# Performance work log

Measured on AMD Instinct MI355X. Metric: run time of the kernel, lower is better.

Reference implementation:

```python
import jax, jax.numpy as jnp
import numpy as np

B, T = 8, 1024
IN_FEAT = 1024
N_FEAT = 1024
N_HEAD = 16
D_K = N_FEAT // N_HEAD
KERNEL = 11
LEFT_PAD = (KERNEL - 1) // 2  # sanm_shift=0
RIGHT_PAD = KERNEL - 1 - LEFT_PAD


def setup_inputs() -> dict:
    key = jax.random.key(0)
    ks = jax.random.split(key, 7)
    hidden_states = jax.random.normal(ks[0], (B, T, IN_FEAT), dtype=jnp.float32)
    mask = jax.random.randint(ks[1], (B, 1, T), 0, 2, dtype=jnp.int32)
    s_qkv = 1.0 / np.sqrt(IN_FEAT)
    s_out = 1.0 / np.sqrt(N_FEAT)
    W_qkv = jax.random.normal(ks[2], (3 * N_FEAT, IN_FEAT), dtype=jnp.float32) * s_qkv
    b_qkv = jnp.zeros((3 * N_FEAT,), dtype=jnp.float32)
    W_out = jax.random.normal(ks[3], (N_FEAT, N_FEAT), dtype=jnp.float32) * s_out
    b_out = jnp.zeros((N_FEAT,), dtype=jnp.float32)
    fsmn_kernel = jax.random.normal(ks[4], (N_FEAT, 1, KERNEL), dtype=jnp.float32) * (1.0 / KERNEL)
    return {"hidden_states": hidden_states, "mask": mask, "W_qkv": W_qkv,
            "b_qkv": b_qkv, "W_out": W_out, "b_out": b_out, "fsmn_kernel": fsmn_kernel}


def _fsmn(v, maskf, fsmn_kernel):
    # v: [B,T,D], maskf: [B,T,1]
    vm = v * maskf
    x = jnp.transpose(vm, (0, 2, 1))  # [B,D,T]
    x = jnp.pad(x, ((0, 0), (0, 0), (LEFT_PAD, RIGHT_PAD)))
    # depthwise conv1d (cross-correlation, matching torch Conv1d)
    y = jax.lax.conv_general_dilated(
        x, fsmn_kernel, window_strides=(1,), padding='VALID',
        dimension_numbers=('NCH', 'OIH', 'NCH'), feature_group_count=N_FEAT)
    y = jnp.transpose(y, (0, 2, 1)) + vm  # [B,T,D]
    return y * maskf


def reference(hidden_states, mask, W_qkv, b_qkv, W_out, b_out, fsmn_kernel):
    b, t, _ = hidden_states.shape
    qkv = jnp.einsum('btf,of->bto', hidden_states, W_qkv) + b_qkv  # [B,T,3*N_FEAT]
    q, k, v = jnp.split(qkv, 3, axis=-1)
    def heads(x):
        return jnp.transpose(x.reshape(b, t, N_HEAD, D_K), (0, 2, 1, 3))  # [B,H,T,D_K]
    q_h, k_h, v_h = heads(q), heads(k), heads(v)

    maskf = mask.reshape(b, t, 1).astype(hidden_states.dtype)
    fsmn_memory = _fsmn(v, maskf, fsmn_kernel)

    scale = D_K ** -0.5
    scores = jnp.einsum('bhqd,bhkd->bhqk', q_h * scale, k_h)  # [B,H,T,T]
    mask_keys = (mask.reshape(b, 1, 1, t) == 0)  # True where padded
    scores = jnp.where(mask_keys, -jnp.inf, scores)
    attn = jax.nn.softmax(scores, axis=-1)
    attn = jnp.where(mask_keys, 0.0, attn)
    ctx = jnp.einsum('bhqk,bhkd->bhqd', attn, v_h)  # [B,H,T,D_K]
    ctx = jnp.transpose(ctx, (0, 2, 1, 3)).reshape(b, t, N_FEAT)
    att_outs = jnp.einsum('btf,of->bto', ctx, W_out) + b_out
    return att_outs + fsmn_memory
```

## Files before the change

kernel.cpp:

```cpp
#include <hip/hip_runtime.h>
#include <stdint.h>


typedef uint16_t u16;
typedef float f32x4 __attribute__((ext_vector_type(4)));
typedef __bf16 bf16x8 __attribute__((ext_vector_type(8)));
typedef __bf16 bf16x2 __attribute__((ext_vector_type(2)));
typedef u16 u16x8 __attribute__((ext_vector_type(8)));
typedef u16 u16x4 __attribute__((ext_vector_type(4)));
typedef short s16x4 __attribute__((ext_vector_type(4)));

__device__ __forceinline__ u16 f2bf(float f) {
    union { float f; uint32_t u; } c; c.f = f;
    uint32_t u = c.u;
    return (u16)((u + 0x7fffu + ((u >> 16) & 1u)) >> 16);
}
__device__ __forceinline__ float bf2f(u16 h) {
    union { uint32_t u; float f; } c; c.u = ((uint32_t)h) << 16;
    return c.f;
}
__device__ __forceinline__ uint32_t pack_bf16(float a, float b) {
    bf16x2 t; t[0] = (__bf16)a; t[1] = (__bf16)b;
    union { bf16x2 v; uint32_t u; } c; c.v = t; return c.u;
}

__global__ __launch_bounds__(256) void cvt_all(const float* __restrict__ hs,
                                               const float* __restrict__ wqkv,
                                               const float* __restrict__ wout,
                                               u16* __restrict__ hsb,
                                               u16* __restrict__ wqkvb,
                                               u16* __restrict__ woutb) {
    int bid = blockIdx.x;
    const float* src; u16* dst; int ib;
    if (bid < 8192)       { src = hs;   dst = hsb;   ib = bid; }
    else if (bid < 11264) { src = wqkv; dst = wqkvb; ib = bid - 8192; }
    else                  { src = wout; dst = woutb; ib = bid - 11264; }
    int i = (ib * 256 + threadIdx.x) * 4;
    float4 v = *reinterpret_cast<const float4*>(src + i);
    ushort4 o;
    o.x = f2bf(v.x); o.y = f2bf(v.y); o.z = f2bf(v.z); o.w = f2bf(v.w);
    *reinterpret_cast<ushort4*>(dst + i) = o;
}

__global__ void mask_and_kt(const int* __restrict__ mask, uint32_t* __restrict__ mb,
                            const float* __restrict__ fk, float* __restrict__ kt) {
    int bid = blockIdx.x;
    if (bid < 44) {
        int idx = bid * 256 + threadIdx.x;
        int j = idx >> 10, c = idx & 1023;
        kt[idx] = fk[c * 11 + j];
    } else {
        int i = threadIdx.x;
        int b = i >> 5, c = i & 31;
        uint32_t u = 0;
        for (int j = 0; j < 32; ++j)
            u |= (mask[(b << 10) + c * 32 + j] ? 1u : 0u) << j;
        mb[i] = u;
    }
}

__global__ __launch_bounds__(256) void transpose_v(const u16* __restrict__ vn,
                                                   u16* __restrict__ vt) {
    __shared__ u16 ts[64][68];
    const int tid = threadIdx.x;
    const int bh = blockIdx.x >> 4;
    const int kc = blockIdx.x & 15;
    const u16* src = vn + ((size_t)bh << 16) + (size_t)kc * 64 * 64;
#pragma unroll
    for (int it = 0; it < 2; ++it) {
        int ch = it * 256 + tid;
        int k = ch >> 3, g = ch & 7;
        *reinterpret_cast<u16x8*>(&ts[k][g * 8]) =
            *reinterpret_cast<const u16x8*>(src + k * 64 + g * 8);
    }
    __syncthreads();
    u16* dst = vt + ((size_t)bh << 16) + kc * 64;
#pragma unroll
    for (int it = 0; it < 2; ++it) {
        int ch = it * 256 + tid;
        int d = ch >> 3, gk = ch & 7;
        u16x8 v;
#pragma unroll
        for (int j = 0; j < 8; ++j) v[j] = ts[gk * 8 + j][d];
        *reinterpret_cast<u16x8*>(dst + (size_t)d * 1024 + gk * 8) = v;
    }
}

template<int MODE>
__global__ __launch_bounds__(512, 4) void gemm_bk32(
    const u16* __restrict__ A, const u16* __restrict__ Bw, int M, int N, int K,
    int ntiles_n, const float* __restrict__ bias,
    u16* __restrict__ qo, u16* __restrict__ ko, u16* __restrict__ vo,
    float* __restrict__ out)
{
    __shared__ u16 lds[36864];
    const int t = threadIdx.x;
    const int lane = t & 63;
    const int wave = t >> 6;
    const int wr = wave >> 2, wc = wave & 3;
    const int lr = lane & 15, lq = lane >> 4;
    const int r3 = lane >> 2, c4 = lane & 3;
    const int cpx = gridDim.x >> 3;
    const int bid = (blockIdx.x & 7) * cpx + (blockIdx.x >> 3);
    const int m0 = (bid / ntiles_n) * 128;
    const int n0 = (bid % ntiles_n) * 256;
    const int NT = K >> 5;

    const u16* AgW  = A  + (size_t)(m0 + wave * 16 + r3) * K + c4 * 8;
    const u16* BgW0 = Bw + (size_t)(n0 + wave * 16 + r3) * K + c4 * 8;
    const u16* BgW1 = BgW0 + (size_t)128 * K;

    auto stage = [&](int buf, int tile) {
        u16* dA  = lds + buf * 12288 + wave * 512;
        u16* dB0 = lds + buf * 12288 + 4096 + wave * 512;
        u16* dB1 = dB0 + 4096;
        __builtin_amdgcn_global_load_lds(
            (const __attribute__((address_space(1))) void*)(AgW + tile * 32),
            (__attribute__((address_space(3))) void*)dA, 16, 0, 0);
        __builtin_amdgcn_global_load_lds(
            (const __attribute__((address_space(1))) void*)(BgW0 + tile * 32),
            (__attribute__((address_space(3))) void*)dB0, 16, 0, 0);
        __builtin_amdgcn_global_load_lds(
            (const __attribute__((address_space(1))) void*)(BgW1 + tile * 32),
            (__attribute__((address_space(3))) void*)dB1, 16, 0, 0);
    };

    f32x4 acc[4][4];
#pragma unroll
    for (int i = 0; i < 4; ++i)
#pragma unroll
        for (int j = 0; j < 4; ++j) acc[i][j] = (f32x4){0.f, 0.f, 0.f, 0.f};

    stage(0, 0);
    stage(1, 1);
    asm volatile("s_waitcnt vmcnt(3)" ::: "memory");
    __builtin_amdgcn_s_barrier();

    for (int T = 0; T < NT; ++T) {
        const int bcur = T % 3;
        const u16* Ab = lds + bcur * 12288;
        const u16* Bb = Ab + 4096;
        bf16x8 a[4], bb[4];
#pragma unroll
        for (int mm = 0; mm < 4; ++mm)
            a[mm] = *reinterpret_cast<const bf16x8*>(Ab + (wr * 64 + mm * 16 + lr) * 32 + lq * 8);
#pragma unroll
        for (int nn = 0; nn < 4; ++nn)
            bb[nn] = *reinterpret_cast<const bf16x8*>(Bb + (wc * 64 + nn * 16 + lr) * 32 + lq * 8);
        if (T + 2 < NT) stage((T + 2) % 3, T + 2);
        __builtin_amdgcn_s_setprio(1);
#pragma unroll
        for (int mm = 0; mm < 4; ++mm)
#pragma unroll
            for (int nn = 0; nn < 4; ++nn)
                acc[mm][nn] = __builtin_amdgcn_mfma_f32_16x16x32_bf16(a[mm], bb[nn], acc[mm][nn], 0, 0, 0);
        __builtin_amdgcn_s_setprio(0);
        if (T + 2 < NT)      asm volatile("s_waitcnt vmcnt(3)" ::: "memory");
        else if (T + 1 < NT) asm volatile("s_waitcnt vmcnt(0)" ::: "memory");
        if (T + 1 < NT) __builtin_amdgcn_s_barrier();
    }

#pragma unroll
    for (int m = 0; m < 4; ++m) {
        int row = m0 + wr * 64 + m * 16 + lq * 4;
#pragma unroll
        for (int n = 0; n < 4; ++n) {
            int col = n0 + wc * 64 + n * 16 + lr;
            float bv = bias[col];
#pragma unroll
            for (int r = 0; r < 4; ++r) {
                float val = acc[m][n][r] + bv;
                int rr = row + r;
                if (MODE == 0) {
                    int part = col >> 10;
                    int cc = col & 1023;
                    int h = cc >> 6, d = cc & 63;
                    int b = rr >> 10, tt = rr & 1023;
                    size_t bh = (size_t)(b * 16 + h);
                    u16* dst = (part == 0) ? qo : (part == 1) ? ko : vo;
                    dst[((bh << 10) + tt) * 64 + d] = f2bf(part == 0 ? val * 0.18033688011f : val);
                } else {
                    size_t o = (size_t)rr * N + col;
                    out[o] += val;
                }
            }
        }
    }
}

__global__ __launch_bounds__(256) void fsmn_v3(const u16* __restrict__ vt,
                                               const int* __restrict__ mask,
                                               const float* __restrict__ kt,
                                               float* __restrict__ out)
{
    __shared__ float vs[64][147];
    __shared__ float ms[144];
    const int tid = threadIdx.x;
    const int tc = blockIdx.x & 7;
    const int bh = blockIdx.x >> 3;
    const int b = bh >> 4, h = bh & 15;
    const int t0 = tc * 128;
    const u16* vrow = vt + ((size_t)bh << 16);
    const int* mrow = mask + (b << 10);

    if (tid < 144) {
        int tt = t0 - 8 + tid;
        ms[tid] = (tt >= 0 && tt < 1024) ? (float)mrow[tt] : 0.f;
    }
    const int sd = tid >> 2;
    const int ci0 = tid & 3;
#pragma unroll
    for (int it = 0; it < 5; ++it) {
        int ci = ci0 + it * 4;
        if (ci < 18) {
            int tbase = t0 - 8 + ci * 8;
            if (tbase >= 0 && tbase < 1024) {
                u16x8 v8 = *reinterpret_cast<const u16x8*>(vrow + (size_t)sd * 1024 + tbase);
#pragma unroll
                for (int j = 0; j < 8; ++j)
                    vs[sd][ci * 8 + j] = bf2f((u16)v8[j]) * (float)mrow[tbase + j];
            } else {
#pragma unroll
                for (int j = 0; j < 8; ++j) vs[sd][ci * 8 + j] = 0.f;
            }
        }
    }
    __syncthreads();

    const int dd = tid & 63;
    const int tg = tid >> 6;
    const int c = h * 64 + dd;
    float kc[11];
#pragma unroll
    for (int j = 0; j < 11; ++j) kc[j] = kt[j * 1024 + c];

    const int tl0 = tg * 32;
    float w[11];
#pragma unroll
    for (int j = 0; j < 11; ++j) w[j] = vs[dd][3 + tl0 + j];
    float* orow = out + ((size_t)(b * 1024 + t0 + tl0)) * 1024 + c;
#pragma unroll 4
    for (int s = 0; s < 32; ++s) {
        float acc = 0.f;
#pragma unroll
        for (int j = 0; j < 11; ++j) acc += kc[j] * w[j];
        float mf = ms[8 + tl0 + s];
        orow[(size_t)s * 1024] = (acc + w[5]) * mf;
#pragma unroll
        for (int j = 0; j < 10; ++j) w[j] = w[j + 1];
        w[10] = vs[dd][3 + tl0 + s + 11];
    }
}

__global__ __launch_bounds__(512) void attn_v9(const u16* __restrict__ qg,
                                               const u16* __restrict__ kg,
                                               const u16* __restrict__ vtg,
                                               const uint32_t* __restrict__ mbits,
                                               u16* __restrict__ ctx)
{
    __shared__ u16 K_s[2][64 * 64];
    __shared__ u16 V_s[2][64 * 64];
    const int t = threadIdx.x;
    const int lane = t & 63;
    const int w = t >> 6;
    const int lr = lane & 15, lq = lane >> 4;
    const int bh = blockIdx.x & 127;
    const int qc = blockIdx.x >> 7;
    const int b = bh >> 4, h = bh & 15;
    const size_t base = (size_t)bh << 16;
    const u16* kb = kg + base;
    const u16* vb = vtg + base;
    const int q0 = qc * 256 + w * 32;

    bf16x8 qf[2][2];
#pragma unroll
    for (int qt = 0; qt < 2; ++qt)
#pragma unroll
        for (int kk = 0; kk < 2; ++kk)
            qf[qt][kk] = *reinterpret_cast<const bf16x8*>(
                qg + base + (size_t)(q0 + qt * 16 + lr) * 64 + kk * 32 + lq * 8);

    f32x4 oacc[2][4];
    f32x4 oacc_l[2];
#pragma unroll
    for (int qt = 0; qt < 2; ++qt) {
        oacc_l[qt] = (f32x4){0.f, 0.f, 0.f, 0.f};
#pragma unroll
        for (int dt = 0; dt < 4; ++dt) oacc[qt][dt] = (f32x4){0.f, 0.f, 0.f, 0.f};
    }

    s16x4 ones_f;
#pragma unroll
    for (int j = 0; j < 4; ++j) ones_f[j] = (short)0x3F80;

    const uint32_t* mrow = mbits + b * 32;

    auto stage = [&](int bufi, int tile) {
        const int k0s = tile * 64;
        int ch = w * 64 + lane;
        int row = ch >> 3, c7 = ch & 7;
        int sc = (c7 ^ (row & 7)) * 8;
        const u16* srcK = kb + (size_t)(k0s + row) * 64 + sc;
        const u16* srcV = vb + (size_t)row * 1024 + k0s + sc;
        u16* dK = &K_s[bufi][(size_t)(w * 64) * 8];
        u16* dV = &V_s[bufi][(size_t)(w * 64) * 8];
        __builtin_amdgcn_global_load_lds(
            (const __attribute__((address_space(1))) void*)srcK,
            (__attribute__((address_space(3))) void*)dK, 16, 0, 0);
        __builtin_amdgcn_global_load_lds(
            (const __attribute__((address_space(1))) void*)srcV,
            (__attribute__((address_space(3))) void*)dV, 16, 0, 0);
    };

    int cur = 0;
    stage(0, 0);
    asm volatile("s_waitcnt vmcnt(0)");
    __syncthreads();

    for (int it = 0; it < 16; ++it) {
        if (it < 15) stage(cur ^ 1, it + 1);

        const u16* Kb = K_s[cur];
        bf16x8 kf[4][2];
#pragma unroll
        for (int kt = 0; kt < 4; ++kt) {
            int row = kt * 16 + lr;
#pragma unroll
            for (int kk = 0; kk < 2; ++kk) {
                int g = (kk * 4 + lq) ^ (row & 7);
                kf[kt][kk] = *reinterpret_cast<const bf16x8*>(Kb + row * 64 + g * 8);
            }
        }

        const uint32_t mw0 = mrow[it * 2], mw1 = mrow[it * 2 + 1];
        uint32_t mb_[4];
        mb_[0] = mw0 >> (lq * 4);
        mb_[1] = mw0 >> (16 + lq * 4);
        mb_[2] = mw1 >> (lq * 4);
        mb_[3] = mw1 >> (16 + lq * 4);
        f32x4 ma[4];
#pragma unroll
        for (int kt = 0; kt < 4; ++kt)
#pragma unroll
            for (int r = 0; r < 4; ++r)
                ma[kt][r] = (mb_[kt] & (1u << r)) ? 0.f : -3e38f;

        const u16* Vb = V_s[cur];
        s16x4 vf[4][4];
#pragma unroll
        for (int ks = 0; ks < 4; ++ks)
#pragma unroll
            for (int dt = 0; dt < 4; ++dt) {
                int row = dt * 16 + lr;
                int g = (ks * 2 + (lq >> 1)) ^ (row & 7);
                vf[ks][dt] = *reinterpret_cast<const s16x4*>(Vb + row * 64 + g * 8 + (lq & 1) * 4);
            }

#pragma unroll
        for (int qt = 0; qt < 2; ++qt) {
            f32x4 s[4];
            __builtin_amdgcn_s_setprio(1);
#pragma unroll
            for (int kt = 0; kt < 4; ++kt) {
                s[kt] = __builtin_amdgcn_mfma_f32_16x16x32_bf16(kf[kt][0], qf[qt][0], ma[kt], 0, 0, 0);
                s[kt] = __builtin_amdgcn_mfma_f32_16x16x32_bf16(kf[kt][1], qf[qt][1], s[kt], 0, 0, 0);
            }
            __builtin_amdgcn_s_setprio(0);

            union { uint32_t u[2]; s16x4 v; } pa[4];
#pragma unroll
            for (int kt = 0; kt < 4; ++kt) {
                float p0 = __builtin_amdgcn_exp2f(s[kt][0]);
                float p1 = __builtin_amdgcn_exp2f(s[kt][1]);
                float p2 = __builtin_amdgcn_exp2f(s[kt][2]);
                float p3 = __builtin_amdgcn_exp2f(s[kt][3]);
                pa[kt].u[0] = pack_bf16(p0, p1);
                pa[kt].u[1] = pack_bf16(p2, p3);
            }

            __builtin_amdgcn_s_setprio(1);
#pragma unroll
            for (int dt = 0; dt < 4; ++dt) {
                f32x4 o = oacc[qt][dt];
#pragma unroll
                for (int kt = 0; kt < 4; ++kt)
                    o = __builtin_amdgcn_mfma_f32_16x16x16bf16_1k(vf[kt][dt], pa[kt].v, o, 0, 0, 0);
                oacc[qt][dt] = o;
            }
#pragma unroll
            for (int kt = 0; kt < 4; ++kt)
                oacc_l[qt] = __builtin_amdgcn_mfma_f32_16x16x16bf16_1k(ones_f, pa[kt].v, oacc_l[qt], 0, 0, 0);
            __builtin_amdgcn_s_setprio(0);
        }

        asm volatile("s_waitcnt vmcnt(0)" ::: "memory");
        __syncthreads();
        cur ^= 1;
    }

#pragma unroll
    for (int qt = 0; qt < 2; ++qt) {
        float li = 1.f / oacc_l[qt][0];
        int trow = q0 + qt * 16 + lr;
        u16* crow = ctx + ((size_t)(b << 10) + trow) * 1024 + h * 64;
#pragma unroll
        for (int dt = 0; dt < 4; ++dt) {
            f32x4 o = oacc[qt][dt];
            u16x4 pkv;
            pkv[0] = f2bf(o[0] * li); pkv[1] = f2bf(o[1] * li);
            pkv[2] = f2bf(o[2] * li); pkv[3] = f2bf(o[3] * li);
            *reinterpret_cast<u16x4*>(crow + dt * 16 + lq * 4) = pkv;
        }
    }
}

extern "C" void kernel_launch(void* const* d_in, const int* in_sizes, int n_in,
                              void* d_out, int out_size, void* d_ws, size_t ws_size,
                              hipStream_t stream)
{
    (void)in_sizes; (void)n_in; (void)out_size; (void)ws_size;
    const float* hs   = (const float*)d_in[0];
    const int*   mask = (const int*)d_in[1];
    const float* Wqkv = (const float*)d_in[2];
    const float* bqkv = (const float*)d_in[3];
    const float* Wout = (const float*)d_in[4];
    const float* bout = (const float*)d_in[5];
    const float* fk   = (const float*)d_in[6];
    float* out = (float*)d_out;

    char* ws = (char*)d_ws;
    u16* hsb   = (u16*)(ws);
    u16* wqkvb = (u16*)(ws + 16777216);
    u16* woutb = (u16*)(ws + 23068672);
    u16* qb    = (u16*)(ws + 25165824);
    u16* kb    = (u16*)(ws + 41943040);
    u16* vtb   = (u16*)(ws + 58720256);
    u16* vnb   = (u16*)(ws + 75497472);
    u16* ctxb  = (u16*)(ws + 75497472);
    uint32_t* mbits = (uint32_t*)ws;
    float* ktT = (float*)(ws + 4096);

    cvt_all<<<12288, 256, 0, stream>>>(hs, Wqkv, Wout, hsb, wqkvb, woutb);

    gemm_bk32<0><<<64 * 12, 512, 0, stream>>>(hsb, wqkvb, 8192, 3072, 1024, 12,
                                              bqkv, qb, kb, vnb, nullptr);
    mask_and_kt<<<45, 256, 0, stream>>>(mask, mbits, fk, ktT);
    transpose_v<<<2048, 256, 0, stream>>>(vnb, vtb);
    fsmn_v3<<<1024, 256, 0, stream>>>(vtb, mask, ktT, out);
    attn_v9<<<512, 512, 0, stream>>>(qb, kb, vtb, mbits, ctxb);
    gemm_bk32<1><<<64 * 4, 512, 0, stream>>>(ctxb, woutb, 8192, 1024, 1024, 4,
                                             bout, nullptr, nullptr, nullptr, out);
}
```

Baseline: 197.8 us.

## Store FSMN output in bf16 scratch, fold into out-proj epilogue; shrink attention blocks

```diff
diff --git a/kernel.cpp b/kernel.cpp
--- a/kernel.cpp
+++ b/kernel.cpp
@@ -181,17 +181,17 @@
                     dst[((bh << 10) + tt) * 64 + d] = f2bf(part == 0 ? val * 0.18033688011f : val);
                 } else {
                     size_t o = (size_t)rr * N + col;
-                    out[o] += val;
+                    out[o] = val + bf2f(vo[o]);
                 }
             }
         }
     }
 }
 
-__global__ __launch_bounds__(256) void fsmn_v3(const u16* __restrict__ vt,
+__global__ __launch_bounds__(256) void fsmn_v4(const u16* __restrict__ vt,
                                                const int* __restrict__ mask,
                                                const float* __restrict__ kt,
-                                               float* __restrict__ out)
+                                               u16* __restrict__ fsb)
 {
     __shared__ float vs[64][147];
     __shared__ float ms[144];
@@ -238,25 +238,25 @@
     float w[11];
 #pragma unroll
     for (int j = 0; j < 11; ++j) w[j] = vs[dd][3 + tl0 + j];
-    float* orow = out + ((size_t)(b * 1024 + t0 + tl0)) * 1024 + c;
+    u16* orow = fsb + ((size_t)(b * 1024 + t0 + tl0)) * 1024 + c;
 #pragma unroll 4
     for (int s = 0; s < 32; ++s) {
         float acc = 0.f;
 #pragma unroll
         for (int j = 0; j < 11; ++j) acc += kc[j] * w[j];
         float mf = ms[8 + tl0 + s];
-        orow[(size_t)s * 1024] = (acc + w[5]) * mf;
+        orow[(size_t)s * 1024] = f2bf((acc + w[5]) * mf);
 #pragma unroll
         for (int j = 0; j < 10; ++j) w[j] = w[j + 1];
         w[10] = vs[dd][3 + tl0 + s + 11];
     }
 }
 
-__global__ __launch_bounds__(512) void attn_v9(const u16* __restrict__ qg,
-                                               const u16* __restrict__ kg,
-                                               const u16* __restrict__ vtg,
-                                               const uint32_t* __restrict__ mbits,
-                                               u16* __restrict__ ctx)
+__global__ __launch_bounds__(256) void attn_v11(const u16* __restrict__ qg,
+                                                const u16* __restrict__ kg,
+                                                const u16* __restrict__ vtg,
+                                                const uint32_t* __restrict__ mbits,
+                                                u16* __restrict__ ctx)
 {
     __shared__ u16 K_s[2][64 * 64];
     __shared__ u16 V_s[2][64 * 64];
@@ -270,7 +270,7 @@
     const size_t base = (size_t)bh << 16;
     const u16* kb = kg + base;
     const u16* vb = vtg + base;
-    const int q0 = qc * 256 + w * 32;
+    const int q0 = qc * 128 + w * 32;
 
     bf16x8 qf[2][2];
 #pragma unroll
@@ -297,30 +297,33 @@
 
     auto stage = [&](int bufi, int tile) {
         const int k0s = tile * 64;
-        int ch = w * 64 + lane;
-        int row = ch >> 3, c7 = ch & 7;
-        int sc = (c7 ^ (row & 7)) * 8;
-        const u16* srcK = kb + (size_t)(k0s + row) * 64 + sc;
-        const u16* srcV = vb + (size_t)row * 1024 + k0s + sc;
-        u16* dK = &K_s[bufi][(size_t)(w * 64) * 8];
-        u16* dV = &V_s[bufi][(size_t)(w * 64) * 8];
-        __builtin_amdgcn_global_load_lds(
-            (const __attribute__((address_space(1))) void*)srcK,
-            (__attribute__((address_space(3))) void*)dK, 16, 0, 0);
-        __builtin_amdgcn_global_load_lds(
-            (const __attribute__((address_space(1))) void*)srcV,
-            (__attribute__((address_space(3))) void*)dV, 16, 0, 0);
+#pragma unroll
+        for (int rd = 0; rd < 2; ++rd) {
+            int ch = rd * 256 + w * 64 + lane;
+            int row = ch >> 3, c7 = ch & 7;
+            int sc = (c7 ^ (row & 7)) * 8;
+            const u16* srcK = kb + (size_t)(k0s + row) * 64 + sc;
+            const u16* srcV = vb + (size_t)row * 1024 + k0s + sc;
+            u16* dK = &K_s[bufi][(size_t)(rd * 256 + w * 64) * 8];
+            u16* dV = &V_s[bufi][(size_t)(rd * 256 + w * 64) * 8];
+            __builtin_amdgcn_global_load_lds(
+                (const __attribute__((address_space(1))) void*)srcK,
+                (__attribute__((address_space(3))) void*)dK, 16, 0, 0);
+            __builtin_amdgcn_global_load_lds(
+                (const __attribute__((address_space(1))) void*)srcV,
+                (__attribute__((address_space(3))) void*)dV, 16, 0, 0);
+        }
     };
 
-    int cur = 0;
     stage(0, 0);
     asm volatile("s_waitcnt vmcnt(0)");
     __syncthreads();
 
     for (int it = 0; it < 16; ++it) {
-        if (it < 15) stage(cur ^ 1, it + 1);
-
-        const u16* Kb = K_s[cur];
+        const u16* Kb = K_s[it & 1];
+        const u16* Vb = V_s[it & 1];
+        if (it < 15) stage((it + 1) & 1, it + 1);
+
         bf16x8 kf[4][2];
 #pragma unroll
         for (int kt = 0; kt < 4; ++kt) {
@@ -345,7 +348,6 @@
             for (int r = 0; r < 4; ++r)
                 ma[kt][r] = (mb_[kt] & (1u << r)) ? 0.f : -3e38f;
 
-        const u16* Vb = V_s[cur];
         s16x4 vf[4][4];
 #pragma unroll
         for (int ks = 0; ks < 4; ++ks)
@@ -393,9 +395,10 @@
             __builtin_amdgcn_s_setprio(0);
         }
 
-        asm volatile("s_waitcnt vmcnt(0)" ::: "memory");
-        __syncthreads();
-        cur ^= 1;
+        if (it < 15) {
+            asm volatile("s_waitcnt vmcnt(0)" ::: "memory");
+            __syncthreads();
+        }
     }
 
 #pragma unroll
@@ -439,6 +442,7 @@
     u16* ctxb  = (u16*)(ws + 75497472);
     uint32_t* mbits = (uint32_t*)ws;
     float* ktT = (float*)(ws + 4096);
+    u16* fsb   = (u16*)(ws + 65536);
 
     cvt_all<<<12288, 256, 0, stream>>>(hs, Wqkv, Wout, hsb, wqkvb, woutb);
 
@@ -446,8 +450,8 @@
                                               bqkv, qb, kb, vnb, nullptr);
     mask_and_kt<<<45, 256, 0, stream>>>(mask, mbits, fk, ktT);
     transpose_v<<<2048, 256, 0, stream>>>(vnb, vtb);
-    fsmn_v3<<<1024, 256, 0, stream>>>(vtb, mask, ktT, out);
-    attn_v9<<<512, 512, 0, stream>>>(qb, kb, vtb, mbits, ctxb);
+    fsmn_v4<<<1024, 256, 0, stream>>>(vtb, mask, ktT, fsb);
+    attn_v11<<<1024, 256, 0, stream>>>(qb, kb, vtb, mbits, ctxb);
     gemm_bk32<1><<<64 * 4, 512, 0, stream>>>(ctxb, woutb, 8192, 1024, 1024, 4,
-                                             bout, nullptr, nullptr, nullptr, out);
-}
+                                             bout, nullptr, nullptr, fsb, out);
+}
```

Result: faster. 187.1 us (-5.4%).
